# Performance work log

Measured on AMD Instinct MI355X. Metric: run time of the kernel, lower is better.

Reference implementation:

```python
import jax, jax.numpy as jnp
from jax import lax
import numpy as np

B = 131072   # batch
M = 16       # in_channel (message dim, m=2^k with k=4)
NCH = 8      # n_channel (complex symbols)
CD = 16      # 2*n_channel
TAPS = 3     # rayleigh channel taps
R = 0.5      # code rate k/n
EBNO = 10.0 ** (7.0 / 10.0)
EPS = 1e-5


def setup_inputs() -> dict:
    ks = jax.random.split(jax.random.key(0), 48)
    f32 = jnp.float32
    def lin(i, o, n):
        return jax.random.normal(ks[i], (o, n), f32) / np.float32(np.sqrt(n))
    def cw(i, o, c, k):
        return jax.random.normal(ks[i], (o, c, k), f32) / np.float32(np.sqrt(c * k))
    def bv(i, n):
        return 0.01 * jax.random.normal(ks[i], (n,), f32)
    return dict(
        x=jax.random.normal(ks[0], (B, M), f32),
        noise=jax.random.normal(ks[1], (B, CD), f32) / np.float32(np.sqrt(2 * R * EBNO)),
        fading=jax.random.normal(ks[2], (B, TAPS, 2), f32),
        ew1=lin(3, M, M), eb1=bv(4, M),
        ew2=lin(5, CD, M), eb2=bv(6, CD),
        ec1w=cw(7, NCH, 1, 2), ec1b=bv(8, NCH),
        ec2w=cw(9, NCH, NCH, 4), ec2b=bv(10, NCH),
        ec3w=cw(11, NCH, NCH, 2), ec3b=bv(12, NCH),
        ec4w=cw(13, NCH, NCH, 2), ec4b=bv(14, NCH),
        ew3=lin(15, CD, 2 * CD), eb3=bv(16, CD),
        bng=jnp.ones((CD,), f32), bnb=jnp.zeros((CD,), f32),
        pw1=lin(17, 2 * CD, CD), pb1=bv(18, 2 * CD),
        pw2=lin(19, 4 * CD, 2 * CD), pb2=bv(20, 4 * CD),
        pw3=lin(21, CD // 2, 4 * CD), pb3=bv(22, CD // 2),
        pw4=lin(23, 2, CD // 2), pb4=bv(24, 2),
        dw1=lin(25, CD, CD), db1=bv(26, CD),
        dc1w=cw(27, NCH, 1, 2), dc1b=bv(28, NCH),
        dc2w=cw(29, NCH, NCH, 4), dc2b=bv(30, NCH),
        dc3w=cw(31, NCH, NCH, 2), dc3b=bv(32, NCH),
        dc4w=cw(33, NCH, NCH, 2), dc4b=bv(34, NCH),
        dw2=lin(35, CD, 2 * CD), db2=bv(36, CD),
        dw3=lin(37, CD, CD), db3=bv(38, CD),
        dw4=lin(39, M, CD), db4=bv(40, M),
    )


def _conv(h, w, bias, s):
    y = lax.conv_general_dilated(h, w, (s,), 'VALID', dimension_numbers=('NCH', 'OIH', 'NCH'))
    return y + bias[None, :, None]


def reference(x, noise, fading, ew1, eb1, ew2, eb2, ec1w, ec1b, ec2w, ec2b, ec3w, ec3b,
              ec4w, ec4b, ew3, eb3, bng, bnb, pw1, pb1, pw2, pb2, pw3, pb3, pw4, pb4,
              dw1, db1, dc1w, dc1b, dc2w, dc2b, dc3w, dc3b, dc4w, dc4b, dw2, db2,
              dw3, db3, dw4, db4):
    elu, tanh = jax.nn.elu, jnp.tanh
    Bn = x.shape[0]
    # ---- encoder ----
    h = elu(x @ ew1.T + eb1)
    h = elu(h @ ew2.T + eb2)                       # (B, CD)
    h = h[:, None, :]                              # (B, 1, CD)
    h = tanh(_conv(h, ec1w, ec1b, 1))              # (B, NCH, 15)
    h = tanh(_conv(h, ec2w, ec2b, 2))              # (B, NCH, 6)
    h = tanh(_conv(h, ec3w, ec3b, 1))              # (B, NCH, 5)
    h = tanh(_conv(h, ec4w, ec4b, 1))              # (B, NCH, 4)
    h = h.reshape(Bn, 2 * bng.shape[0])            # (B, 2*CD)
    h = h @ ew3.T + eb3                            # (B, CD)
    mu = h.mean(0)
    var = h.var(0)                                 # biased var (torch BN training mode)
    enc = (h - mu) / jnp.sqrt(var + EPS) * bng + bnb
    # ---- rayleigh multipath channel: vectorized complex FIR over taps ----
    taps = fading.shape[1]
    xc = enc.reshape(Bn, -1, 2)                    # (B, NCH, 2) re/im pairs
    n_sym = xc.shape[1]
    pad = taps - 1
    padded = jnp.pad(xc, ((0, 0), (pad, pad), (0, 0)))
    idx = jnp.arange(n_sym + taps - 1)[:, None] + jnp.arange(taps)[None, :]
    win = padded[:, idx]                           # (B, L_out, taps, 2)
    ff = fading[:, ::-1]                           # per-example flipped taps
    yr = jnp.einsum('blt,bt->bl', win[..., 0], ff[..., 0]) - jnp.einsum('blt,bt->bl', win[..., 1], ff[..., 1])
    yi = jnp.einsum('blt,bt->bl', win[..., 0], ff[..., 1]) + jnp.einsum('blt,bt->bl', win[..., 1], ff[..., 0])
    y = jnp.stack([yr, yi], -1)[:, :n_sym]         # drop trailing taps-1 samples
    c = y.reshape(Bn, 2 * n_sym) + noise
    # ---- channel parameter estimation ----
    p = elu(c @ pw1.T + pb1)
    p = tanh(p @ pw2.T + pb2)
    p = tanh(p @ pw3.T + pb3)
    hp = p @ pw4.T + pb4                           # (B, 2) estimated complex h
    # ---- transform: complex division x / h ----
    cc = c.reshape(Bn, n_sym, 2)
    hr, hi = hp[:, 0:1], hp[:, 1:2]
    den = hr * hr + hi * hi
    tr = (cc[..., 0] * hr + cc[..., 1] * hi) / den
    ti = (cc[..., 1] * hr - cc[..., 0] * hi) / den
    t = jnp.stack([tr, ti], -1).reshape(Bn, 2 * n_sym)
    # ---- decoder ----
    d = tanh(t @ dw1.T + db1)
    d = d[:, None, :]
    d = tanh(_conv(d, dc1w, dc1b, 1))
    d = tanh(_conv(d, dc2w, dc2b, 2))
    d = tanh(_conv(d, dc3w, dc3b, 1))
    d = tanh(_conv(d, dc4w, dc4b, 1))
    d = d.reshape(Bn, -1)
    d = tanh(d @ dw2.T + db2)
    d = tanh(d @ dw3.T + db3)
    return d @ dw4.T + db4
```

## Files before the change

kernel.cpp:

```cpp
#include <hip/hip_runtime.h>


#define BTOT 131072
#define BLK  256
#define NBLK 512
#define NW   6768

constexpr int EW1 = 0;     constexpr int EB1 = 256;
constexpr int EW2 = 272;   constexpr int EB2 = 528;
constexpr int EC1W = 544;  constexpr int EC1B = 560;
constexpr int EC2W = 568;  constexpr int EC2B = 824;
constexpr int EC3W = 832;  constexpr int EC3B = 960;
constexpr int EC4W = 968;  constexpr int EC4B = 1096;
constexpr int EW3 = 1104;  constexpr int EB3 = 1616;
constexpr int BNG = 1632;  constexpr int BNB = 1648;
constexpr int PW1 = 1664;  constexpr int PB1 = 2176;
constexpr int PW2 = 2208;  constexpr int PB2 = 4256;
constexpr int PW3 = 4320;  constexpr int PB3 = 4832;
constexpr int PW4 = 4840;  constexpr int PB4 = 4856;
constexpr int DW1 = 4864;  constexpr int DB1 = 5120;
constexpr int DC1W = 5136; constexpr int DC1B = 5152;
constexpr int DC2W = 5160; constexpr int DC2B = 5416;
constexpr int DC3W = 5424; constexpr int DC3B = 5552;
constexpr int DC4W = 5560; constexpr int DC4B = 5688;
constexpr int DW2 = 5696;  constexpr int DB2 = 6208;
constexpr int DW3 = 6224;  constexpr int DB3 = 6480;
constexpr int DW4 = 6496;  constexpr int DB4 = 6752;

constexpr size_t WS_W    = 0;
constexpr size_t WS_BAR  = 28672;
constexpr size_t WS_DONE = 28800;
constexpr size_t WS_SCSH = 28928;
constexpr size_t WS_PART = 32768;

__device__ __forceinline__ float bf2f(unsigned int u) {
  union { unsigned int i; float f; } v; v.i = u << 16; return v.f;
}
__device__ __forceinline__ unsigned short f2bf(float f) {
  union { float f; unsigned int i; } v; v.f = f;
  unsigned int x = v.i;
  return (unsigned short)((x + 0x7fffu + ((x >> 16) & 1u)) >> 16);
}
__device__ __forceinline__ void unpack8(uint4 u, float* f) {
  f[0] = bf2f(u.x & 0xffffu); f[1] = bf2f(u.x >> 16);
  f[2] = bf2f(u.y & 0xffffu); f[3] = bf2f(u.y >> 16);
  f[4] = bf2f(u.z & 0xffffu); f[5] = bf2f(u.z >> 16);
  f[6] = bf2f(u.w & 0xffffu); f[7] = bf2f(u.w >> 16);
}
__device__ __forceinline__ int sniff_bf16(const void* bng) {
  return *(const unsigned int*)bng != 0x3F800000u;
}
__device__ __forceinline__ void load16(const void* base, int b, int isbf, float* f) {
  if (isbf) {
    const uint4* p = (const uint4*)((const unsigned short*)base + (size_t)b * 16);
    unpack8(p[0], f); unpack8(p[1], f + 8);
  } else {
    const float4* p = (const float4*)((const float*)base + (size_t)b * 16);
#pragma unroll
    for (int q = 0; q < 4; q++) {
      float4 v = p[q];
      f[4 * q] = v.x; f[4 * q + 1] = v.y; f[4 * q + 2] = v.z; f[4 * q + 3] = v.w;
    }
  }
}
__device__ __forceinline__ void store16(void* base, int b, int isbf, const float* f) {
  if (isbf) {
    unsigned int ov[8];
#pragma unroll
    for (int j = 0; j < 8; j++)
      ov[j] = (unsigned int)f2bf(f[2 * j]) | ((unsigned int)f2bf(f[2 * j + 1]) << 16);
    uint4* op = (uint4*)((unsigned short*)base + (size_t)b * 16);
    op[0] = make_uint4(ov[0], ov[1], ov[2], ov[3]);
    op[1] = make_uint4(ov[4], ov[5], ov[6], ov[7]);
  } else {
    float4* op = (float4*)((float*)base + (size_t)b * 16);
#pragma unroll
    for (int q = 0; q < 4; q++)
      op[q] = make_float4(f[4 * q], f[4 * q + 1], f[4 * q + 2], f[4 * q + 3]);
  }
}
__device__ __forceinline__ float tanh_f(float x) {
  float e = __expf(2.0f * x);
  return 1.0f - 2.0f * __builtin_amdgcn_rcpf(e + 1.0f);
}
__device__ __forceinline__ float elu_f(float x) {
  return x > 0.0f ? x : __expf(x) - 1.0f;
}

template <int OUT, int IN, int WOFF, int BOFF, int ACT>
__device__ __forceinline__ void dense1(const float* w, const float* in, float* out) {
#pragma unroll
  for (int m = 0; m < OUT; m++) {
    float v = w[BOFF + m];
#pragma unroll
    for (int k = 0; k < IN; k += 4) {
      float4 wv = *(const float4*)(w + WOFF + m * IN + k);
      v += in[k] * wv.x; v += in[k + 1] * wv.y;
      v += in[k + 2] * wv.z; v += in[k + 3] * wv.w;
    }
    if (ACT == 1) v = elu_f(v);
    if (ACT == 2) v = tanh_f(v);
    out[m] = v;
  }
}

template <int W1, int B1, int W2, int B2, int W3, int B3, int W4, int B4>
__device__ __forceinline__ void conv_chain1(const float* w, const float h[16],
                                            float flat[32]) {
  float c1[4][8];
  float c2[6][8];
#pragma unroll
  for (int p = 0; p < 6; p++) {
    const int p0 = (p == 0) ? 0 : (2 * p + 2);
#pragma unroll
    for (int pos = p0; pos <= 2 * p + 3; ++pos) {
#pragma unroll
      for (int o = 0; o < 8; o++) {
        float2 wv = *(const float2*)(w + W1 + o * 2);
        float v = h[pos] * wv.x + h[pos + 1] * wv.y + w[B1 + o];
        c1[pos & 3][o] = tanh_f(v);
      }
    }
#pragma unroll
    for (int o = 0; o < 8; o++) {
      float v = w[B2 + o];
#pragma unroll
      for (int i = 0; i < 8; i++) {
        float4 wv = *(const float4*)(w + W2 + (o * 8 + i) * 4);
        v += c1[(2 * p) & 3][i] * wv.x;
        v += c1[(2 * p + 1) & 3][i] * wv.y;
        v += c1[(2 * p + 2) & 3][i] * wv.z;
        v += c1[(2 * p + 3) & 3][i] * wv.w;
      }
      c2[p][o] = tanh_f(v);
    }
  }
  float c3[5][8];
#pragma unroll
  for (int p = 0; p < 5; p++) {
#pragma unroll
    for (int o = 0; o < 8; o++) {
      float v = w[B3 + o];
#pragma unroll
      for (int i = 0; i < 8; i++) {
        float2 wv = *(const float2*)(w + W3 + (o * 8 + i) * 2);
        v += c2[p][i] * wv.x + c2[p + 1][i] * wv.y;
      }
      c3[p][o] = tanh_f(v);
    }
  }
#pragma unroll
  for (int p = 0; p < 4; p++) {
#pragma unroll
    for (int o = 0; o < 8; o++) {
      float v = w[B4 + o];
#pragma unroll
      for (int i = 0; i < 8; i++) {
        float2 wv = *(const float2*)(w + W4 + (o * 8 + i) * 2);
        v += c3[p][i] * wv.x + c3[p + 1][i] * wv.y;
      }
      flat[o * 4 + p] = tanh_f(v);
    }
  }
}

struct Segs {
  const void* src[40];
  int cnt[40];
  int off[40];
};

__global__ __launch_bounds__(256) void k_convert(Segs s, const void* __restrict__ bng_src,
                                                 float* __restrict__ dst,
                                                 unsigned int* __restrict__ bar,
                                                 unsigned int* __restrict__ done) {
  if (blockIdx.x == 0 && threadIdx.x == 0) {
    __hip_atomic_store(bar, 0u, __ATOMIC_RELAXED, __HIP_MEMORY_SCOPE_AGENT);
    __hip_atomic_store(done, 0u, __ATOMIC_RELAXED, __HIP_MEMORY_SCOPE_AGENT);
  }
  const int isbf = sniff_bf16(bng_src);
  const int seg = blockIdx.x;
  const int n = s.cnt[seg];
  const int o = s.off[seg];
  if (isbf) {
    const unsigned short* p = (const unsigned short*)s.src[seg];
    for (int i = threadIdx.x; i < n; i += 256) dst[o + i] = bf2f((unsigned int)p[i]);
  } else {
    const float* p = (const float*)s.src[seg];
    for (int i = threadIdx.x; i < n; i += 256) dst[o + i] = p[i];
  }
}

__global__ __launch_bounds__(BLK, 2) void k_fused(const void* __restrict__ x,
                                                  const void* __restrict__ noise,
                                                  const void* __restrict__ fading,
                                                  const void* __restrict__ bng_src,
                                                  const float* __restrict__ wg,
                                                  float* __restrict__ partials,
                                                  unsigned int* __restrict__ bar,
                                                  unsigned int* __restrict__ done,
                                                  float* __restrict__ scsh_ws,
                                                  void* __restrict__ out) {
  const int isbf = sniff_bf16(bng_src);
  const int b = blockIdx.x * BLK + threadIdx.x;

  float xv[16];
  load16(x, b, isbf, xv);

  __shared__ float sw[NW];
  for (int i = threadIdx.x; i < NW / 4; i += BLK)
    ((float4*)sw)[i] = ((const float4*)wg)[i];
  __syncthreads();

  __shared__ float he_lds[16][BLK];

  {
    float he[16];
    {
      float h1[16], h2[16];
      dense1<16, 16, EW1, EB1, 1>(sw, xv, h1);
      dense1<16, 16, EW2, EB2, 1>(sw, h1, h2);
      float flat[32];
      conv_chain1<EC1W, EC1B, EC2W, EC2B, EC3W, EC3B, EC4W, EC4B>(sw, h2, flat);
      dense1<16, 32, EW3, EB3, 0>(sw, flat, he);
    }

#pragma unroll
    for (int j = 0; j < 16; j++) he_lds[j][threadIdx.x] = he[j];

    __shared__ float part[4][32];
    const int lane = threadIdx.x & 63;
    const int wid = threadIdx.x >> 6;
#pragma unroll
    for (int j = 0; j < 16; j++) {
      float s = he[j];
      float q = he[j] * he[j];
#pragma unroll
      for (int m = 32; m >= 1; m >>= 1) {
        s += __shfl_xor(s, m, 64);
        q += __shfl_xor(q, m, 64);
      }
      if (lane == 0) { part[wid][j] = s; part[wid][16 + j] = q; }
    }
    __syncthreads();
    if (threadIdx.x < 32)
      __hip_atomic_store(&partials[blockIdx.x * 32 + threadIdx.x],
                         part[0][threadIdx.x] + part[1][threadIdx.x] +
                             part[2][threadIdx.x] + part[3][threadIdx.x],
                         __ATOMIC_RELAXED, __HIP_MEMORY_SCOPE_AGENT);
    __syncthreads();
  }

  __shared__ unsigned int sh_master;
  __shared__ float scl[32];
  if (threadIdx.x == 0) {
    unsigned int old = __hip_atomic_fetch_add(bar, 1u, __ATOMIC_RELAXED,
                                              __HIP_MEMORY_SCOPE_AGENT);
    sh_master = (old == (unsigned int)(NBLK - 1)) ? 1u : 0u;
  }
  __syncthreads();

  if (sh_master) {
    __threadfence();
    const int ch = threadIdx.x & 31;
    const int g = threadIdx.x >> 5;
    const float* pp = partials + g * 2048 + ch;
    float a0 = 0, a1 = 0, a2 = 0, a3 = 0;
#pragma unroll 2
    for (int k = 0; k < 64; k += 4) {
      a0 += pp[(k + 0) * 32];
      a1 += pp[(k + 1) * 32];
      a2 += pp[(k + 2) * 32];
      a3 += pp[(k + 3) * 32];
    }
    __shared__ float red[8][32];
    red[g][ch] = (a0 + a1) + (a2 + a3);
    __syncthreads();
    __shared__ float tot[32];
    if (threadIdx.x < 32) {
      float v = 0.0f;
#pragma unroll
      for (int g2 = 0; g2 < 8; g2++) v += red[g2][threadIdx.x];
      tot[threadIdx.x] = v;
    }
    __syncthreads();
    if (threadIdx.x < 16) {
      const float invB = 1.0f / (float)BTOT;
      float mu = tot[threadIdx.x] * invB;
      float var = tot[16 + threadIdx.x] * invB - mu * mu;
      float rstd = rsqrtf(var + 1e-5f);
      float sc = sw[BNG + threadIdx.x] * rstd;
      scl[threadIdx.x] = sc;
      scl[16 + threadIdx.x] = sw[BNB + threadIdx.x] - mu * sc;
    }
    __syncthreads();
    if (threadIdx.x < 32)
      __hip_atomic_store(&scsh_ws[threadIdx.x], scl[threadIdx.x],
                         __ATOMIC_RELAXED, __HIP_MEMORY_SCOPE_AGENT);
    __syncthreads();
    if (threadIdx.x == 0)
      __hip_atomic_store(done, 1u, __ATOMIC_RELEASE, __HIP_MEMORY_SCOPE_AGENT);
  } else {
    if (threadIdx.x == 0) {
      while (__hip_atomic_load(done, __ATOMIC_RELAXED,
                               __HIP_MEMORY_SCOPE_AGENT) == 0u)
        __builtin_amdgcn_s_sleep(16);
    }
    __syncthreads();
    if (threadIdx.x < 32)
      scl[threadIdx.x] = __hip_atomic_load(&scsh_ws[threadIdx.x],
                                           __ATOMIC_RELAXED,
                                           __HIP_MEMORY_SCOPE_AGENT);
  }
  __syncthreads();

  float nz[16];
  load16(noise, b, isbf, nz);
  float fr[3], fi[3];
  if (isbf) {
    const unsigned int* fa =
        (const unsigned int*)((const unsigned short*)fading + (size_t)b * 6);
#pragma unroll
    for (int j = 0; j < 3; j++) {
      unsigned int ua = fa[j];
      fr[j] = bf2f(ua & 0xffffu); fi[j] = bf2f(ua >> 16);
    }
  } else {
    const float2* fa = (const float2*)((const float*)fading + (size_t)b * 6);
#pragma unroll
    for (int j = 0; j < 3; j++) {
      float2 a = fa[j];
      fr[j] = a.x; fi[j] = a.y;
    }
  }

  float he[16];
#pragma unroll
  for (int j = 0; j < 16; j++) {
    he[j] = he_lds[j][threadIdx.x] * scl[j] + scl[16 + j];
  }

  float c[16];
#pragma unroll
  for (int l = 0; l < 8; l++) {
    float ar = 0.0f, ai = 0.0f;
#pragma unroll
    for (int j = 0; j < 3; j++) {
      if (l - j >= 0) {
        float xr = he[2 * (l - j)], xi = he[2 * (l - j) + 1];
        ar += xr * fr[j] - xi * fi[j];
        ai += xr * fi[j] + xi * fr[j];
      }
    }
    c[2 * l] = ar + nz[2 * l];
    c[2 * l + 1] = ai + nz[2 * l + 1];
  }
  float p1[32];
  dense1<32, 16, PW1, PB1, 1>(sw, c, p1);
  float p3[8];
#pragma unroll
  for (int j = 0; j < 8; j++) p3[j] = sw[PB3 + j];
#pragma unroll
  for (int n0 = 0; n0 < 64; n0 += 4) {
    float tv[4];
#pragma unroll
    for (int u = 0; u < 4; u++) {
      const int n = n0 + u;
      float v = sw[PB2 + n];
#pragma unroll
      for (int k = 0; k < 32; k += 4) {
        float4 wv = *(const float4*)(sw + PW2 + n * 32 + k);
        v += p1[k] * wv.x; v += p1[k + 1] * wv.y;
        v += p1[k + 2] * wv.z; v += p1[k + 3] * wv.w;
      }
      tv[u] = tanh_f(v);
    }
#pragma unroll
    for (int j = 0; j < 8; j++) {
      float4 wv = *(const float4*)(sw + PW3 + j * 64 + n0);
      p3[j] += tv[0] * wv.x + tv[1] * wv.y + tv[2] * wv.z + tv[3] * wv.w;
    }
  }
#pragma unroll
  for (int j = 0; j < 8; j++) p3[j] = tanh_f(p3[j]);
  float hr = sw[PB4 + 0], hi = sw[PB4 + 1];
#pragma unroll
  for (int k = 0; k < 8; k++) {
    hr += p3[k] * sw[PW4 + k];
    hi += p3[k] * sw[PW4 + 8 + k];
  }
  float den = hr * hr + hi * hi;
  float inv = __builtin_amdgcn_rcpf(den);
  float tt[16];
#pragma unroll
  for (int l = 0; l < 8; l++) {
    float c0 = c[2 * l], c1v = c[2 * l + 1];
    tt[2 * l] = (c0 * hr + c1v * hi) * inv;
    tt[2 * l + 1] = (c1v * hr - c0 * hi) * inv;
  }
  float d1[16];
  dense1<16, 16, DW1, DB1, 2>(sw, tt, d1);
  float flat[32];
  conv_chain1<DC1W, DC1B, DC2W, DC2B, DC3W, DC3B, DC4W, DC4B>(sw, d1, flat);
  float d2[16], d3[16], o[16];
  dense1<16, 32, DW2, DB2, 2>(sw, flat, d2);
  dense1<16, 16, DW3, DB3, 2>(sw, d2, d3);
  dense1<16, 16, DW4, DB4, 0>(sw, d3, o);

  store16(out, b, isbf, o);
}

extern "C" void kernel_launch(void* const* d_in, const int* in_sizes, int n_in,
                              void* d_out, int out_size, void* d_ws, size_t ws_size,
                              hipStream_t stream) {
  float* wbuf = (float*)((char*)d_ws + WS_W);
  float* partials = (float*)((char*)d_ws + WS_PART);
  unsigned int* bar = (unsigned int*)((char*)d_ws + WS_BAR);
  unsigned int* done = (unsigned int*)((char*)d_ws + WS_DONE);
  float* scsh_ws = (float*)((char*)d_ws + WS_SCSH);

  static const int offs[40] = {
      EW1, EB1, EW2, EB2, EC1W, EC1B, EC2W, EC2B, EC3W, EC3B, EC4W, EC4B,
      EW3, EB3, BNG, BNB, PW1, PB1, PW2, PB2, PW3, PB3, PW4, PB4,
      DW1, DB1, DC1W, DC1B, DC2W, DC2B, DC3W, DC3B, DC4W, DC4B,
      DW2, DB2, DW3, DB3, DW4, DB4};
  Segs segs;
  for (int k = 0; k < 40; k++) {
    segs.src[k] = d_in[3 + k];
    segs.cnt[k] = in_sizes[3 + k];
    segs.off[k] = offs[k];
  }
  const void* bng_src = d_in[17];

  k_convert<<<40, 256, 0, stream>>>(segs, bng_src, wbuf, bar, done);
  k_fused<<<NBLK, BLK, 0, stream>>>(d_in[0], d_in[1], d_in[2], bng_src, wbuf,
                                    partials, bar, done, scsh_ws, d_out);
}
```

Baseline: 247.1 us.

## Split fused kernel at batchnorm into encoder and main kernels with atomic stats

Replaces the single persistent kernel that used a grid-wide spin barrier with two kernels. The encoder kernel writes its pre-batchnorm activations to the output buffer and atomically accumulates per-channel sums. The main kernel then reads the sums, computes the batchnorm scale and shift, and runs the rest of the network. This removes the spin-wait and the single-block reduction, and lets the encoder use a smaller weight copy in shared memory. In exchange it adds a global round-trip of the intermediate activations, stored in bf16 when inputs are bf16, which may lose precision. Float atomic accumulation also makes the result order-dependent, and block size changes to 128.

```diff
diff --git a/kernel.cpp b/kernel.cpp
--- a/kernel.cpp
+++ b/kernel.cpp
@@ -2,9 +2,10 @@
 
 
 #define BTOT 131072
-#define BLK  256
-#define NBLK 512
+#define BLK  128
+#define NBLK 1024
 #define NW   6768
+#define NW_E 1632
 
 constexpr int EW1 = 0;     constexpr int EB1 = 256;
 constexpr int EW2 = 272;   constexpr int EB2 = 528;
@@ -27,11 +28,8 @@
 constexpr int DW3 = 6224;  constexpr int DB3 = 6480;
 constexpr int DW4 = 6496;  constexpr int DB4 = 6752;
 
-constexpr size_t WS_W    = 0;
-constexpr size_t WS_BAR  = 28672;
-constexpr size_t WS_DONE = 28800;
-constexpr size_t WS_SCSH = 28928;
-constexpr size_t WS_PART = 32768;
+constexpr size_t WS_W   = 0;
+constexpr size_t WS_ACC = 28672;
 
 __device__ __forceinline__ float bf2f(unsigned int u) {
   union { unsigned int i; float f; } v; v.i = u << 16; return v.f;
@@ -172,12 +170,10 @@
 
 __global__ __launch_bounds__(256) void k_convert(Segs s, const void* __restrict__ bng_src,
                                                  float* __restrict__ dst,
-                                                 unsigned int* __restrict__ bar,
-                                                 unsigned int* __restrict__ done) {
-  if (blockIdx.x == 0 && threadIdx.x == 0) {
-    __hip_atomic_store(bar, 0u, __ATOMIC_RELAXED, __HIP_MEMORY_SCOPE_AGENT);
-    __hip_atomic_store(done, 0u, __ATOMIC_RELAXED, __HIP_MEMORY_SCOPE_AGENT);
-  }
+                                                 float* __restrict__ accum) {
+  if (blockIdx.x == 0 && threadIdx.x < 32)
+    __hip_atomic_store(&accum[threadIdx.x], 0.0f, __ATOMIC_RELAXED,
+                       __HIP_MEMORY_SCOPE_AGENT);
   const int isbf = sniff_bf16(bng_src);
   const int seg = blockIdx.x;
   const int n = s.cnt[seg];
@@ -191,129 +187,66 @@
   }
 }
 
-__global__ __launch_bounds__(BLK, 2) void k_fused(const void* __restrict__ x,
-                                                  const void* __restrict__ noise,
-                                                  const void* __restrict__ fading,
-                                                  const void* __restrict__ bng_src,
-                                                  const float* __restrict__ wg,
-                                                  float* __restrict__ partials,
-                                                  unsigned int* __restrict__ bar,
-                                                  unsigned int* __restrict__ done,
-                                                  float* __restrict__ scsh_ws,
-                                                  void* __restrict__ out) {
+__global__ __launch_bounds__(BLK, 1) void k_enc(const void* __restrict__ x,
+                                                const void* __restrict__ bng_src,
+                                                const float* __restrict__ wg,
+                                                float* __restrict__ accum,
+                                                void* __restrict__ outbuf) {
   const int isbf = sniff_bf16(bng_src);
   const int b = blockIdx.x * BLK + threadIdx.x;
 
   float xv[16];
   load16(x, b, isbf, xv);
 
-  __shared__ float sw[NW];
-  for (int i = threadIdx.x; i < NW / 4; i += BLK)
+  __shared__ float sw[NW_E];
+  for (int i = threadIdx.x; i < NW_E / 4; i += BLK)
     ((float4*)sw)[i] = ((const float4*)wg)[i];
   __syncthreads();
 
-  __shared__ float he_lds[16][BLK];
-
+  float he[16];
   {
-    float he[16];
-    {
-      float h1[16], h2[16];
-      dense1<16, 16, EW1, EB1, 1>(sw, xv, h1);
-      dense1<16, 16, EW2, EB2, 1>(sw, h1, h2);
-      float flat[32];
-      conv_chain1<EC1W, EC1B, EC2W, EC2B, EC3W, EC3B, EC4W, EC4B>(sw, h2, flat);
-      dense1<16, 32, EW3, EB3, 0>(sw, flat, he);
-    }
-
-#pragma unroll
-    for (int j = 0; j < 16; j++) he_lds[j][threadIdx.x] = he[j];
-
-    __shared__ float part[4][32];
-    const int lane = threadIdx.x & 63;
-    const int wid = threadIdx.x >> 6;
-#pragma unroll
-    for (int j = 0; j < 16; j++) {
-      float s = he[j];
-      float q = he[j] * he[j];
-#pragma unroll
-      for (int m = 32; m >= 1; m >>= 1) {
-        s += __shfl_xor(s, m, 64);
-        q += __shfl_xor(q, m, 64);
-      }
-      if (lane == 0) { part[wid][j] = s; part[wid][16 + j] = q; }
-    }
-    __syncthreads();
-    if (threadIdx.x < 32)
-      __hip_atomic_store(&partials[blockIdx.x * 32 + threadIdx.x],
-                         part[0][threadIdx.x] + part[1][threadIdx.x] +
-                             part[2][threadIdx.x] + part[3][threadIdx.x],
-                         __ATOMIC_RELAXED, __HIP_MEMORY_SCOPE_AGENT);
-    __syncthreads();
-  }
-
-  __shared__ unsigned int sh_master;
-  __shared__ float scl[32];
-  if (threadIdx.x == 0) {
-    unsigned int old = __hip_atomic_fetch_add(bar, 1u, __ATOMIC_RELAXED,
-                                              __HIP_MEMORY_SCOPE_AGENT);
-    sh_master = (old == (unsigned int)(NBLK - 1)) ? 1u : 0u;
+    float h1[16], h2[16];
+    dense1<16, 16, EW1, EB1, 1>(sw, xv, h1);
+    dense1<16, 16, EW2, EB2, 1>(sw, h1, h2);
+    float flat[32];
+    conv_chain1<EC1W, EC1B, EC2W, EC2B, EC3W, EC3B, EC4W, EC4B>(sw, h2, flat);
+    dense1<16, 32, EW3, EB3, 0>(sw, flat, he);
+  }
+
+  store16(outbuf, b, isbf, he);
+
+  __shared__ float part[2][32];
+  const int lane = threadIdx.x & 63;
+  const int wid = threadIdx.x >> 6;
+#pragma unroll
+  for (int j = 0; j < 16; j++) {
+    float s = he[j];
+    float q = he[j] * he[j];
+#pragma unroll
+    for (int m = 32; m >= 1; m >>= 1) {
+      s += __shfl_xor(s, m, 64);
+      q += __shfl_xor(q, m, 64);
+    }
+    if (lane == 0) { part[wid][j] = s; part[wid][16 + j] = q; }
   }
   __syncthreads();
-
-  if (sh_master) {
-    __threadfence();
-    const int ch = threadIdx.x & 31;
-    const int g = threadIdx.x >> 5;
-    const float* pp = partials + g * 2048 + ch;
-    float a0 = 0, a1 = 0, a2 = 0, a3 = 0;
-#pragma unroll 2
-    for (int k = 0; k < 64; k += 4) {
-      a0 += pp[(k + 0) * 32];
-      a1 += pp[(k + 1) * 32];
-      a2 += pp[(k + 2) * 32];
-      a3 += pp[(k + 3) * 32];
-    }
-    __shared__ float red[8][32];
-    red[g][ch] = (a0 + a1) + (a2 + a3);
-    __syncthreads();
-    __shared__ float tot[32];
-    if (threadIdx.x < 32) {
-      float v = 0.0f;
-#pragma unroll
-      for (int g2 = 0; g2 < 8; g2++) v += red[g2][threadIdx.x];
-      tot[threadIdx.x] = v;
-    }
-    __syncthreads();
-    if (threadIdx.x < 16) {
-      const float invB = 1.0f / (float)BTOT;
-      float mu = tot[threadIdx.x] * invB;
-      float var = tot[16 + threadIdx.x] * invB - mu * mu;
-      float rstd = rsqrtf(var + 1e-5f);
-      float sc = sw[BNG + threadIdx.x] * rstd;
-      scl[threadIdx.x] = sc;
-      scl[16 + threadIdx.x] = sw[BNB + threadIdx.x] - mu * sc;
-    }
-    __syncthreads();
-    if (threadIdx.x < 32)
-      __hip_atomic_store(&scsh_ws[threadIdx.x], scl[threadIdx.x],
-                         __ATOMIC_RELAXED, __HIP_MEMORY_SCOPE_AGENT);
-    __syncthreads();
-    if (threadIdx.x == 0)
-      __hip_atomic_store(done, 1u, __ATOMIC_RELEASE, __HIP_MEMORY_SCOPE_AGENT);
-  } else {
-    if (threadIdx.x == 0) {
-      while (__hip_atomic_load(done, __ATOMIC_RELAXED,
-                               __HIP_MEMORY_SCOPE_AGENT) == 0u)
-        __builtin_amdgcn_s_sleep(16);
-    }
-    __syncthreads();
-    if (threadIdx.x < 32)
-      scl[threadIdx.x] = __hip_atomic_load(&scsh_ws[threadIdx.x],
-                                           __ATOMIC_RELAXED,
-                                           __HIP_MEMORY_SCOPE_AGENT);
-  }
-  __syncthreads();
-
+  if (threadIdx.x < 32)
+    __hip_atomic_fetch_add(&accum[threadIdx.x],
+                           part[0][threadIdx.x] + part[1][threadIdx.x],
+                           __ATOMIC_RELAXED, __HIP_MEMORY_SCOPE_AGENT);
+}
+
+__global__ __launch_bounds__(BLK, 1) void k_main(const void* __restrict__ noise,
+                                                 const void* __restrict__ fading,
+                                                 const void* __restrict__ bng_src,
+                                                 const float* __restrict__ wg,
+                                                 const float* __restrict__ accum,
+                                                 void* __restrict__ out) {
+  const int isbf = sniff_bf16(bng_src);
+  const int b = blockIdx.x * BLK + threadIdx.x;
+
+  float hev[16];
+  load16(out, b, isbf, hev);
   float nz[16];
   load16(noise, b, isbf, nz);
   float fr[3], fi[3];
@@ -334,11 +267,31 @@
     }
   }
 
+  __shared__ float sw[NW];
+  for (int i = threadIdx.x; i < NW / 4; i += BLK)
+    ((float4*)sw)[i] = ((const float4*)wg)[i];
+
+  __shared__ float tot[32];
+  __shared__ float scl[32];
+  if (threadIdx.x < 32)
+    tot[threadIdx.x] = __hip_atomic_load(&accum[threadIdx.x],
+                                         __ATOMIC_RELAXED,
+                                         __HIP_MEMORY_SCOPE_AGENT);
+  __syncthreads();
+  if (threadIdx.x < 16) {
+    const float invB = 1.0f / (float)BTOT;
+    float mu = tot[threadIdx.x] * invB;
+    float var = tot[16 + threadIdx.x] * invB - mu * mu;
+    float rstd = rsqrtf(var + 1e-5f);
+    float sc = sw[BNG + threadIdx.x] * rstd;
+    scl[threadIdx.x] = sc;
+    scl[16 + threadIdx.x] = sw[BNB + threadIdx.x] - mu * sc;
+  }
+  __syncthreads();
+
   float he[16];
 #pragma unroll
-  for (int j = 0; j < 16; j++) {
-    he[j] = he_lds[j][threadIdx.x] * scl[j] + scl[16 + j];
-  }
+  for (int j = 0; j < 16; j++) he[j] = hev[j] * scl[j] + scl[16 + j];
 
   float c[16];
 #pragma unroll
@@ -414,10 +367,7 @@
                               void* d_out, int out_size, void* d_ws, size_t ws_size,
                               hipStream_t stream) {
   float* wbuf = (float*)((char*)d_ws + WS_W);
-  float* partials = (float*)((char*)d_ws + WS_PART);
-  unsigned int* bar = (unsigned int*)((char*)d_ws + WS_BAR);
-  unsigned int* done = (unsigned int*)((char*)d_ws + WS_DONE);
-  float* scsh_ws = (float*)((char*)d_ws + WS_SCSH);
+  float* accum = (float*)((char*)d_ws + WS_ACC);
 
   static const int offs[40] = {
       EW1, EB1, EW2, EB2, EC1W, EC1B, EC2W, EC2B, EC3W, EC3B, EC4W, EC4B,
@@ -432,7 +382,7 @@
   }
   const void* bng_src = d_in[17];
 
-  k_convert<<<40, 256, 0, stream>>>(segs, bng_src, wbuf, bar, done);
-  k_fused<<<NBLK, BLK, 0, stream>>>(d_in[0], d_in[1], d_in[2], bng_src, wbuf,
-                                    partials, bar, done, scsh_ws, d_out);
-}
+  k_convert<<<40, 256, 0, stream>>>(segs, bng_src, wbuf, accum);
+  k_enc<<<NBLK, BLK, 0, stream>>>(d_in[0], bng_src, wbuf, accum, d_out);
+  k_main<<<NBLK, BLK, 0, stream>>>(d_in[1], d_in[2], bng_src, wbuf, accum, d_out);
+}
```

New measurement: 283.0 us. +14.5%, slower.
